# Kernel optimization log

Hardware: AMD Instinct MI355X
Metric: run time of the kernel (lower is better)

## Reference

```python
import jax, jax.numpy as jnp
import numpy as np


def kmax_dmp(x, pool_ranges, k_per, K):
    """Vectorized dynamic k-max pooling (order-preserving top-k along time).

    x: [B, T, C] float. pool_ranges: [B] int (per-sample valid prefix length).
    k_per: [B] int (per-sample k, k_per[i] <= pool_ranges[i]). K: static max k.
    Returns [B, K, C]; rows beyond k_per[i] are zero-padded (like pad_sequence).
    """
    B, T, C = x.shape
    neg = jnp.finfo(x.dtype).min
    valid = jnp.arange(T)[None, :] < pool_ranges[:, None]            # [B,T]
    xm = jnp.where(valid[:, :, None], x, neg)
    vals, idx = jax.lax.top_k(jnp.swapaxes(xm, 1, 2), K)             # [B,C,K]
    keep = jnp.arange(K)[None, None, :] < k_per[:, None, None]       # [B,1,K] bcast
    idx = jnp.where(keep, idx, T)                                    # sentinel for dropped slots
    order = jnp.argsort(idx, axis=-1)                                # restore temporal order
    vals = jnp.take_along_axis(vals, order, axis=-1)
    idx = jnp.take_along_axis(idx, order, axis=-1)
    vals = jnp.where(idx < T, vals, jnp.zeros((), x.dtype))          # zero-pad tail
    return jnp.swapaxes(vals, 1, 2)                                  # [B,K,C]


def setup_inputs() -> dict:
    key = jax.random.key(0)
    ks = jax.random.split(key, 8)
    B, T, C = 64, 512, 300
    x = jax.random.normal(ks[0], (B, T, C), jnp.float32)
    lengths = jnp.sort(jax.random.randint(ks[1], (B,), 16, T + 1))[::-1]
    lengths = lengths.at[0].set(T)  # packed sequences are sorted desc; max len == T
    w1 = jax.random.normal(ks[2], (3 * C, 2, 7), jnp.float32) * 0.05        # groups=C//2 -> 2 in-ch/group
    b1 = jax.random.normal(ks[3], (3 * C,), jnp.float32) * 0.05
    w2 = jax.random.normal(ks[4], (14 * C // 4, 2, 6, 5), jnp.float32) * 0.05  # groups=C//4 -> 2 in-ch/group
    b2 = jax.random.normal(ks[5], (14 * C // 4,), jnp.float32) * 0.05
    wfc = jax.random.normal(ks[6], (1, 4 * 14 * C // 4), jnp.float32) * 0.05
    bfc = jax.random.normal(ks[7], (1,), jnp.float32) * 0.05
    return {"x": x, "lengths": lengths, "w1": w1, "b1": b1,
            "w2": w2, "b2": b2, "wfc": wfc, "bfc": bfc}


def reference(x, lengths, w1, b1, w2, b2, wfc, bfc):
    B, T, C = x.shape
    G1, G2 = C // 2, C // 4
    TOP_K, KS1, KS2W = 4, 7, 5
    # zero out padded tail (pad_packed_sequence semantics)
    mask = (jnp.arange(T)[None, :] < lengths[:, None]).astype(x.dtype)
    x = x * mask[:, :, None]
    # grouped conv1d: [B,C,T] -> [B,3C,T+6]
    h = jax.lax.conv_general_dilated(
        jnp.swapaxes(x, 1, 2), w1, (1,), [(KS1 - 1, KS1 - 1)],
        dimension_numbers=("NCH", "OIH", "NCH"), feature_group_count=G1)
    h = h + b1[None, :, None]
    h = jnp.swapaxes(h, 1, 2)                                       # [B,T+6,3C]
    # layer-1 dynamic k-max: k_i = max(top_k, ceil((2-1)/2 * len_i))
    k1 = jnp.maximum(TOP_K, (lengths + 1) // 2)
    K1 = max(TOP_K, (T + 1) // 2)                                   # static (max len == T)
    h = kmax_dmp(h, lengths + (KS1 - 1), k1, K1)                    # [B,K1,3C]
    h = jnp.tanh(jnp.swapaxes(h, 1, 2).reshape(B, G1, 6, K1))       # [B,C//2,6,K1]
    # grouped conv2d: -> [B,14*C//4,1,K1+4]
    h = jax.lax.conv_general_dilated(
        h, w2, (1, 1), [(0, 0), (KS2W - 1, KS2W - 1)],
        dimension_numbers=("NCHW", "OIHW", "NCHW"), feature_group_count=G2)
    h = h + b2[None, :, None, None]
    Wd = K1 + KS2W - 1
    h = h.reshape(B, G2, 14, Wd).transpose(0, 3, 2, 1)              # [B,Wd,14,C//4]
    h = h.reshape(B, Wd, 14 * G2)
    # layer-2 dynamic k-max: k = top_k = 4; valid prefix = k1 + 4
    h = kmax_dmp(h, k1 + (KS2W - 1), jnp.full((B,), TOP_K, lengths.dtype), TOP_K)
    h = jnp.tanh(h).reshape(B, -1)                                  # [B,4*14*C//4]
    out = h @ wfc.T + bfc                                           # [B,1]
    return jnp.concatenate([jnp.zeros_like(out), out], axis=1)      # [B,2]
```

## Files before the change

kernel.cpp:

```cpp
#include <hip/hip_runtime.h>
#include <cstdint>
#include <cstddef>

#define BB   64
#define TT   512
#define CC   300
#define NG1  150
#define OC1  900
#define L1   518
#define K1   256
#define NG2  75
#define W2LEN 260

__device__ __forceinline__ unsigned f2key(float f) {
    unsigned u = __float_as_uint(f);
    return (u & 0x80000000u) ? ~u : (u | 0x80000000u);
}

__global__ void init_out(const float* __restrict__ bfc, float* __restrict__ out) {
    int i = threadIdx.x;
    if (i < 2 * BB) out[i] = (i & 1) ? bfc[0] : 0.0f;
}

__global__ __launch_bounds__(384) void conv1_kmax(
    const float* __restrict__ x, const int* __restrict__ lengths,
    const float* __restrict__ w1, const float* __restrict__ b1,
    float* __restrict__ y1)
{
    const int g   = blockIdx.x;
    const int b   = blockIdx.y;
    const int tid = threadIdx.x;
    const int len = lengths[b];
    const int n   = len + 6;
    const int k   = max(4, (len + 1) >> 1);

    __shared__ float xs[2][524];
    __shared__ float hrow[6][584];
    __shared__ float ws1[84];
    __shared__ float bs1[6];

    if (tid < 84) ws1[tid] = w1[g * 84 + tid];
    if (tid < 6)  bs1[tid] = b1[g * 6 + tid];

    for (int p = tid; p < 2 * 524; p += 384) {
        int ic = p / 524, q = p - ic * 524;
        int t  = q - 6;
        float v = 0.0f;
        if (t >= 0 && t < len) v = x[((size_t)b * TT + t) * CC + (2 * g + ic)];
        xs[ic][q] = v;
    }
    __syncthreads();

    for (int i = tid; i < 6 * L1; i += 384) {
        int r = i / L1, t = i - r * L1;
        if (t < n) {
            float acc = bs1[r];
            #pragma unroll
            for (int ic = 0; ic < 2; ++ic)
                #pragma unroll
                for (int kk = 0; kk < 7; ++kk)
                    acc = fmaf(xs[ic][t + kk], ws1[r * 14 + ic * 7 + kk], acc);
            hrow[r][t] = acc;
        }
    }
    __syncthreads();

    const int r    = tid >> 6;
    const int lane = tid & 63;

    float    v[9];
    unsigned key[9];
    #pragma unroll
    for (int j = 0; j < 9; ++j) {
        int  t     = lane + 64 * j;
        bool valid = (t < n);
        float vv   = hrow[r][t];
        v[j]   = valid ? vv : 0.0f;
        key[j] = valid ? f2key(vv) : 0u;
    }

    unsigned lo = 1u, hi = 0xFFFFFFFFu;
    while (lo < hi) {
        unsigned mid = lo + ((hi - lo + 1) >> 1);
        int c = 0;
        #pragma unroll
        for (int j = 0; j < 9; ++j) c += (key[j] >= mid) ? 1 : 0;
        for (int o = 32; o; o >>= 1) c += __shfl_xor(c, o);
        if (c >= k) lo = mid; else hi = mid - 1;
    }
    const unsigned tau = lo;

    int cg = 0;
    #pragma unroll
    for (int j = 0; j < 9; ++j) cg += (key[j] > tau) ? 1 : 0;
    for (int o = 32; o; o >>= 1) cg += __shfl_xor(cg, o);
    const int budget = k - cg;

    float* outrow = y1 + ((size_t)(b * OC1 + g * 6 + r)) * K1;
    const unsigned long long below = (1ull << lane) - 1ull;

    int baseG = 0, baseE = 0;
    #pragma unroll
    for (int j = 0; j < 9; ++j) {
        bool isG = key[j] > tau;
        bool isE = (key[j] == tau);
        unsigned long long mG = __ballot(isG);
        unsigned long long mE = __ballot(isE);
        int A = baseG + __popcll(mG & below);
        int E = baseE + __popcll(mE & below);
        if (isG || (isE && E < budget)) {
            int pos = A + (E < budget ? E : budget);
            outrow[pos] = tanhf(v[j]);
        }
        baseG += __popcll(mG);
        baseE += __popcll(mE);
    }
    for (int w = k + lane; w < K1; w += 64) outrow[w] = 0.0f;
}

__global__ __launch_bounds__(256) void conv2_kmax_fc(
    const float* __restrict__ y1, const int* __restrict__ lengths,
    const float* __restrict__ w2, const float* __restrict__ b2,
    const float* __restrict__ wfc, float* __restrict__ out)
{
    const int g   = blockIdx.x;
    const int b   = blockIdx.y;
    const int tid = threadIdx.x;
    const int len = lengths[b];
    const int k1  = max(4, (len + 1) >> 1);
    const int n2  = k1 + 4;

    __shared__ float ys[12][264];
    __shared__ float hs[14][264];
    __shared__ float ws2[14 * 60];
    __shared__ float bs2[14];
    __shared__ float partial[14];

    for (int i = tid; i < 14 * 60; i += 256) ws2[i] = w2[(size_t)g * 840 + i];
    if (tid < 14) bs2[tid] = b2[g * 14 + tid];

    for (int i = tid; i < 12 * 264; i += 256) {
        int c = i / 264, p = i - c * 264;
        int w = p - 4;
        float vv = 0.0f;
        if (w >= 0 && w < K1) vv = y1[((size_t)(b * OC1 + g * 12 + c)) * K1 + w];
        ys[c][p] = vv;
    }
    __syncthreads();

    for (int i = tid; i < 14 * W2LEN; i += 256) {
        int r2 = i / W2LEN, w = i - r2 * W2LEN;
        if (w < n2) {
            float acc = bs2[r2];
            #pragma unroll
            for (int c = 0; c < 12; ++c)
                #pragma unroll
                for (int kw = 0; kw < 5; ++kw)
                    acc = fmaf(ys[c][w + kw], ws2[r2 * 60 + c * 5 + kw], acc);
            hs[r2][w] = acc;
        }
    }
    __syncthreads();

    if (tid < 14) {
        const int r2 = tid;
        float tv0 = -INFINITY, tv1 = -INFINITY, tv2 = -INFINITY, tv3 = -INFINITY;
        int   ti0 = 1 << 30,   ti1 = 1 << 30,   ti2 = 1 << 30,   ti3 = 1 << 30;
        for (int w = 0; w < n2; ++w) {
            float vv = hs[r2][w];
            if (vv > tv3) {
                if (vv > tv0)      { tv3=tv2; ti3=ti2; tv2=tv1; ti2=ti1; tv1=tv0; ti1=ti0; tv0=vv; ti0=w; }
                else if (vv > tv1) { tv3=tv2; ti3=ti2; tv2=tv1; ti2=ti1; tv1=vv; ti1=w; }
                else if (vv > tv2) { tv3=tv2; ti3=ti2; tv2=vv; ti2=w; }
                else               { tv3=vv; ti3=w; }
            }
        }
        #define CSWAP(a,bq) if (ti##a > ti##bq) { int t_=ti##a; ti##a=ti##bq; ti##bq=t_; float f_=tv##a; tv##a=tv##bq; tv##bq=f_; }
        CSWAP(0,1) CSWAP(2,3) CSWAP(0,2) CSWAP(1,3) CSWAP(1,2)
        #undef CSWAP
        const int f = r2 * 75 + g;
        float s = 0.0f;
        s += tanhf(tv0) * wfc[0 * 1050 + f];
        s += tanhf(tv1) * wfc[1 * 1050 + f];
        s += tanhf(tv2) * wfc[2 * 1050 + f];
        s += tanhf(tv3) * wfc[3 * 1050 + f];
        partial[r2] = s;
    }
    __syncthreads();

    if (tid == 0) {
        float s = 0.0f;
        #pragma unroll
        for (int i = 0; i < 14; ++i) s += partial[i];
        atomicAdd(&out[b * 2 + 1], s);
    }
}

extern "C" void kernel_launch(void* const* d_in, const int* in_sizes, int n_in,
                              void* d_out, int out_size, void* d_ws, size_t ws_size,
                              hipStream_t stream) {
    const float* x       = (const float*)d_in[0];
    const int*   lengths = (const int*)  d_in[1];
    const float* w1      = (const float*)d_in[2];
    const float* b1      = (const float*)d_in[3];
    const float* w2      = (const float*)d_in[4];
    const float* b2      = (const float*)d_in[5];
    const float* wfc     = (const float*)d_in[6];
    const float* bfc     = (const float*)d_in[7];
    float* out = (float*)d_out;
    float* y1  = (float*)d_ws;

    init_out<<<dim3(1), dim3(128), 0, stream>>>(bfc, out);
    conv1_kmax<<<dim3(NG1, BB), dim3(384), 0, stream>>>(x, lengths, w1, b1, y1);
    conv2_kmax_fc<<<dim3(NG2, BB), dim3(256), 0, stream>>>(y1, lengths, w2, b2, wfc, out);
}
```

Measured before the change: 397.7 us.

## Register-resident conv1/conv2 with float-bisection k-max and wave-parallel top-4 selection

Conv1 now computes each output row in registers, with every lane handling S consecutive timesteps loaded via float4. The k-max threshold is found by bisection on float values bounded by the row min and max, with an early exit, instead of a 32-step bisection over integer keys. Conv2 drops its shared-memory staging: each wave loads padded y1 rows (stride 264, zero-padded) straight from global memory and accumulates 4 outputs × 4 channels in registers. Its top-4 selection becomes a wave-wide argmax reduction instead of serial selection on 14 threads. Fast tanh approximations and per-wave atomics reduce the remaining overhead, at some precision risk and more atomic traffic.

Measured after the change: 335.1 us. -15.7%, faster.

```diff
diff --git a/kernel.cpp b/kernel.cpp
--- a/kernel.cpp
+++ b/kernel.cpp
@@ -7,19 +7,143 @@
 #define CC   300
 #define NG1  150
 #define OC1  900
-#define L1   518
 #define K1   256
+#define RS   264
 #define NG2  75
-#define W2LEN 260
 
 __device__ __forceinline__ unsigned f2key(float f) {
     unsigned u = __float_as_uint(f);
     return (u & 0x80000000u) ? ~u : (u | 0x80000000u);
 }
+__device__ __forceinline__ float key2f(unsigned k) {
+    unsigned u = (k & 0x80000000u) ? (k & 0x7FFFFFFFu) : ~k;
+    return __uint_as_float(u);
+}
+__device__ __forceinline__ float fast_tanh(float x) {
+    float e = __expf(2.0f * x);
+    return 1.0f - 2.0f * __builtin_amdgcn_rcpf(e + 1.0f);
+}
+__device__ __forceinline__ int mbcnt64(unsigned long long m) {
+    return (int)__builtin_amdgcn_mbcnt_hi((unsigned)(m >> 32),
+                 __builtin_amdgcn_mbcnt_lo((unsigned)m, 0u));
+}
 
 __global__ void init_out(const float* __restrict__ bfc, float* __restrict__ out) {
     int i = threadIdx.x;
     if (i < 2 * BB) out[i] = (i & 1) ? bfc[0] : 0.0f;
+}
+
+template<int S>
+__device__ __forceinline__ void conv1_core(
+    const float (* __restrict__ xs)[524], int lane, int n, int k,
+    const float* wA, const float* wB, float br, float* __restrict__ row)
+{
+    constexpr int NV = (S == 8) ? 16 : 12;
+    const int t0 = S * lane;
+
+    float xa[NV], xb[NV];
+    #pragma unroll
+    for (int q = 0; q < NV / 4; ++q) {
+        *(float4*)&xa[4 * q] = *(const float4*)&xs[0][t0 + 4 * q];
+        *(float4*)&xb[4 * q] = *(const float4*)&xs[1][t0 + 4 * q];
+    }
+
+    float v[S + 1];
+    #pragma unroll
+    for (int j = 0; j < S; ++j) {
+        float acc = br;
+        #pragma unroll
+        for (int kk = 0; kk < 7; ++kk)
+            acc = fmaf(xa[j + kk], wA[kk], fmaf(xb[j + kk], wB[kk], acc));
+        v[j] = (t0 + j < n) ? acc : -INFINITY;
+    }
+    v[S] = -INFINITY;
+    if (S == 8 && n > 512) {
+        if (lane < 6 && 512 + lane < n) {
+            float acc = br;
+            #pragma unroll
+            for (int kk = 0; kk < 7; ++kk)
+                acc = fmaf(xs[0][512 + lane + kk], wA[kk],
+                      fmaf(xs[1][512 + lane + kk], wB[kk], acc));
+            v[S] = acc;
+        }
+    }
+
+    float lmax = -INFINITY, lmin = INFINITY;
+    #pragma unroll
+    for (int j = 0; j <= S; ++j) {
+        lmax = fmaxf(lmax, v[j]);
+        lmin = fminf(lmin, (v[j] == -INFINITY) ? INFINITY : v[j]);
+    }
+    #pragma unroll
+    for (int o = 32; o; o >>= 1) {
+        lmax = fmaxf(lmax, __shfl_xor(lmax, o));
+        lmin = fminf(lmin, __shfl_xor(lmin, o));
+    }
+    const float vmax = lmax, vmin = lmin;
+
+    float tau; bool found = false;
+    int cmax = 0;
+    #pragma unroll
+    for (int j = 0; j <= S; ++j) cmax += (int)__popcll(__ballot(v[j] == vmax));
+    if (cmax >= k) {
+        tau = vmax;
+    } else {
+        float lo = vmin, hi = vmax;
+        tau = lo;
+        while (true) {
+            float mid = 0.5f * (lo + hi);
+            if (mid == lo || mid == hi) { tau = lo; break; }
+            int c = 0;
+            #pragma unroll
+            for (int j = 0; j <= S; ++j)
+                c += (int)__popcll(__ballot(v[j] >= mid));
+            if (c == k) { tau = mid; found = true; break; }
+            if (c > k) lo = mid; else hi = mid;
+        }
+    }
+
+    bool bG[S + 1], bE[S + 1];
+    unsigned long long mG[S + 1], mE[S + 1];
+    #pragma unroll
+    for (int j = 0; j <= S; ++j) {
+        bG[j] = found ? (v[j] >= tau) : (v[j] > tau);
+        bE[j] = found ? false : (v[j] == tau);
+        mG[j] = __ballot(bG[j]);
+        mE[j] = __ballot(bE[j]);
+    }
+    int cg = 0;
+    #pragma unroll
+    for (int j = 0; j <= S; ++j) cg += (int)__popcll(mG[j]);
+    const int budget = k - cg;
+
+    int SGm = 0, SEm = 0, FGm = 0, FEm = 0;
+    #pragma unroll
+    for (int j = 0; j < S; ++j) {
+        SGm += mbcnt64(mG[j]);  FGm += (int)__popcll(mG[j]);
+        SEm += mbcnt64(mE[j]);  FEm += (int)__popcll(mE[j]);
+    }
+    int ownG = 0, ownE = 0;
+    #pragma unroll
+    for (int j = 0; j < S; ++j) {
+        if (bG[j] || bE[j]) {
+            int E = SEm + ownE;
+            if (bG[j] || E < budget) {
+                int pos = SGm + ownG + min(E, budget);
+                row[4 + pos] = fast_tanh(v[j]);
+            }
+        }
+        ownG += bG[j] ? 1 : 0;  ownE += bE[j] ? 1 : 0;
+    }
+    if (S == 8 && (bG[S] || bE[S])) {
+        int E = FEm + mbcnt64(mE[S]);
+        if (bG[S] || E < budget) {
+            int pos = FGm + mbcnt64(mG[S]) + min(E, budget);
+            row[4 + pos] = fast_tanh(v[S]);
+        }
+    }
+    if (lane < 4) row[lane] = 0.0f;
+    for (int w = k + lane; w < RS - 4; w += 64) row[4 + w] = 0.0f;
 }
 
 __global__ __launch_bounds__(384) void conv1_kmax(
@@ -27,95 +151,34 @@
     const float* __restrict__ w1, const float* __restrict__ b1,
     float* __restrict__ y1)
 {
-    const int g   = blockIdx.x;
-    const int b   = blockIdx.y;
+    const int g = blockIdx.x, b = blockIdx.y;
     const int tid = threadIdx.x;
     const int len = lengths[b];
-    const int n   = len + 6;
-    const int k   = max(4, (len + 1) >> 1);
-
-    __shared__ float xs[2][524];
-    __shared__ float hrow[6][584];
-    __shared__ float ws1[84];
-    __shared__ float bs1[6];
-
-    if (tid < 84) ws1[tid] = w1[g * 84 + tid];
-    if (tid < 6)  bs1[tid] = b1[g * 6 + tid];
-
-    for (int p = tid; p < 2 * 524; p += 384) {
-        int ic = p / 524, q = p - ic * 524;
-        int t  = q - 6;
-        float v = 0.0f;
-        if (t >= 0 && t < len) v = x[((size_t)b * TT + t) * CC + (2 * g + ic)];
-        xs[ic][q] = v;
+    const int n = len + 6;
+    const int k = max(4, (len + 1) >> 1);
+
+    __shared__ __align__(16) float xs[2][524];
+    __shared__ float ws[84];
+    __shared__ float bs[6];
+    if (tid < 84) ws[tid] = w1[g * 84 + tid];
+    if (tid < 6)  bs[tid] = b1[g * 6 + tid];
+    for (int p = tid; p < 1048; p += 384) {
+        int ic = (p >= 524) ? 1 : 0;
+        int q = p - ic * 524;
+        int t = q - 6;
+        xs[ic][q] = (t >= 0 && t < len) ? x[((size_t)b * TT + t) * CC + 2 * g + ic] : 0.0f;
     }
     __syncthreads();
 
-    for (int i = tid; i < 6 * L1; i += 384) {
-        int r = i / L1, t = i - r * L1;
-        if (t < n) {
-            float acc = bs1[r];
-            #pragma unroll
-            for (int ic = 0; ic < 2; ++ic)
-                #pragma unroll
-                for (int kk = 0; kk < 7; ++kk)
-                    acc = fmaf(xs[ic][t + kk], ws1[r * 14 + ic * 7 + kk], acc);
-            hrow[r][t] = acc;
-        }
-    }
-    __syncthreads();
-
-    const int r    = tid >> 6;
-    const int lane = tid & 63;
-
-    float    v[9];
-    unsigned key[9];
-    #pragma unroll
-    for (int j = 0; j < 9; ++j) {
-        int  t     = lane + 64 * j;
-        bool valid = (t < n);
-        float vv   = hrow[r][t];
-        v[j]   = valid ? vv : 0.0f;
-        key[j] = valid ? f2key(vv) : 0u;
-    }
-
-    unsigned lo = 1u, hi = 0xFFFFFFFFu;
-    while (lo < hi) {
-        unsigned mid = lo + ((hi - lo + 1) >> 1);
-        int c = 0;
-        #pragma unroll
-        for (int j = 0; j < 9; ++j) c += (key[j] >= mid) ? 1 : 0;
-        for (int o = 32; o; o >>= 1) c += __shfl_xor(c, o);
-        if (c >= k) lo = mid; else hi = mid - 1;
-    }
-    const unsigned tau = lo;
-
-    int cg = 0;
-    #pragma unroll
-    for (int j = 0; j < 9; ++j) cg += (key[j] > tau) ? 1 : 0;
-    for (int o = 32; o; o >>= 1) cg += __shfl_xor(cg, o);
-    const int budget = k - cg;
-
-    float* outrow = y1 + ((size_t)(b * OC1 + g * 6 + r)) * K1;
-    const unsigned long long below = (1ull << lane) - 1ull;
-
-    int baseG = 0, baseE = 0;
-    #pragma unroll
-    for (int j = 0; j < 9; ++j) {
-        bool isG = key[j] > tau;
-        bool isE = (key[j] == tau);
-        unsigned long long mG = __ballot(isG);
-        unsigned long long mE = __ballot(isE);
-        int A = baseG + __popcll(mG & below);
-        int E = baseE + __popcll(mE & below);
-        if (isG || (isE && E < budget)) {
-            int pos = A + (E < budget ? E : budget);
-            outrow[pos] = tanhf(v[j]);
-        }
-        baseG += __popcll(mG);
-        baseE += __popcll(mE);
-    }
-    for (int w = k + lane; w < K1; w += 64) outrow[w] = 0.0f;
+    const int r = tid >> 6, lane = tid & 63;
+    float wA[7], wB[7];
+    #pragma unroll
+    for (int i = 0; i < 7; ++i) { wA[i] = ws[r * 14 + i]; wB[i] = ws[r * 14 + 7 + i]; }
+    const float br = bs[r];
+    float* row = y1 + ((size_t)b * OC1 + g * 6 + r) * RS;
+
+    if (n <= 256) conv1_core<4>(xs, lane, n, k, wA, wB, br, row);
+    else          conv1_core<8>(xs, lane, n, k, wA, wB, br, row);
 }
 
 __global__ __launch_bounds__(256) void conv2_kmax_fc(
@@ -123,77 +186,128 @@
     const float* __restrict__ w2, const float* __restrict__ b2,
     const float* __restrict__ wfc, float* __restrict__ out)
 {
-    const int g   = blockIdx.x;
-    const int b   = blockIdx.y;
+    const int g = blockIdx.x, b = blockIdx.y;
     const int tid = threadIdx.x;
+    const int wv = tid >> 6, lane = tid & 63;
     const int len = lengths[b];
-    const int k1  = max(4, (len + 1) >> 1);
-    const int n2  = k1 + 4;
-
-    __shared__ float ys[12][264];
-    __shared__ float hs[14][264];
-    __shared__ float ws2[14 * 60];
-    __shared__ float bs2[14];
-    __shared__ float partial[14];
-
-    for (int i = tid; i < 14 * 60; i += 256) ws2[i] = w2[(size_t)g * 840 + i];
-    if (tid < 14) bs2[tid] = b2[g * 14 + tid];
-
-    for (int i = tid; i < 12 * 264; i += 256) {
-        int c = i / 264, p = i - c * 264;
-        int w = p - 4;
-        float vv = 0.0f;
-        if (w >= 0 && w < K1) vv = y1[((size_t)(b * OC1 + g * 12 + c)) * K1 + w];
-        ys[c][p] = vv;
-    }
-    __syncthreads();
-
-    for (int i = tid; i < 14 * W2LEN; i += 256) {
-        int r2 = i / W2LEN, w = i - r2 * W2LEN;
-        if (w < n2) {
-            float acc = bs2[r2];
-            #pragma unroll
-            for (int c = 0; c < 12; ++c)
-                #pragma unroll
-                for (int kw = 0; kw < 5; ++kw)
-                    acc = fmaf(ys[c][w + kw], ws2[r2 * 60 + c * 5 + kw], acc);
-            hs[r2][w] = acc;
-        }
-    }
-    __syncthreads();
-
-    if (tid < 14) {
-        const int r2 = tid;
-        float tv0 = -INFINITY, tv1 = -INFINITY, tv2 = -INFINITY, tv3 = -INFINITY;
-        int   ti0 = 1 << 30,   ti1 = 1 << 30,   ti2 = 1 << 30,   ti3 = 1 << 30;
-        for (int w = 0; w < n2; ++w) {
-            float vv = hs[r2][w];
-            if (vv > tv3) {
-                if (vv > tv0)      { tv3=tv2; ti3=ti2; tv2=tv1; ti2=ti1; tv1=tv0; ti1=ti0; tv0=vv; ti0=w; }
-                else if (vv > tv1) { tv3=tv2; ti3=ti2; tv2=tv1; ti2=ti1; tv1=vv; ti1=w; }
-                else if (vv > tv2) { tv3=tv2; ti3=ti2; tv2=vv; ti2=w; }
-                else               { tv3=vv; ti3=w; }
+    const int k1 = max(4, (len + 1) >> 1);
+    const int n2 = k1 + 4;
+
+    const int r2u0 = __builtin_amdgcn_readfirstlane(4 * wv);
+    const int nch  = (wv == 3) ? 2 : 4;
+    const float* __restrict__ wg = w2 + (size_t)g * 840;
+    const float* base = y1 + ((size_t)b * OC1 + g * 12) * RS;
+
+    float bias_s[4];
+    #pragma unroll
+    for (int it = 0; it < 4; ++it)
+        bias_s[it] = (4 * wv + it < 14) ? b2[(size_t)g * 14 + r2u0 + it] : 0.0f;
+
+    float acc[4][4];
+    #pragma unroll
+    for (int it = 0; it < 4; ++it)
+        #pragma unroll
+        for (int j = 0; j < 4; ++j) acc[it][j] = bias_s[it];
+
+    for (int c = 0; c < 12; ++c) {
+        const float* rp = base + (size_t)c * RS;
+        const float4 f0 = *(const float4*)&rp[4 * lane];
+        const float4 f1 = *(const float4*)&rp[4 * lane + 4];
+        const float e[8] = {f0.x, f0.y, f0.z, f0.w, f1.x, f1.y, f1.z, f1.w};
+        #pragma unroll
+        for (int it = 0; it < 4; ++it) {
+            if (it < nch) {
+                const float* wp = wg + (r2u0 + it) * 60 + c * 5;
+                #pragma unroll
+                for (int kw = 0; kw < 5; ++kw) {
+                    const float q = wp[kw];
+                    acc[it][0] = fmaf(e[0 + kw], q, acc[it][0]);
+                    acc[it][1] = fmaf(e[1 + kw], q, acc[it][1]);
+                    acc[it][2] = fmaf(e[2 + kw], q, acc[it][2]);
+                    acc[it][3] = fmaf(e[3 + kw], q, acc[it][3]);
+                }
             }
         }
-        #define CSWAP(a,bq) if (ti##a > ti##bq) { int t_=ti##a; ti##a=ti##bq; ti##bq=t_; float f_=tv##a; tv##a=tv##bq; tv##bq=f_; }
-        CSWAP(0,1) CSWAP(2,3) CSWAP(0,2) CSWAP(1,3) CSWAP(1,2)
-        #undef CSWAP
-        const int f = r2 * 75 + g;
-        float s = 0.0f;
-        s += tanhf(tv0) * wfc[0 * 1050 + f];
-        s += tanhf(tv1) * wfc[1 * 1050 + f];
-        s += tanhf(tv2) * wfc[2 * 1050 + f];
-        s += tanhf(tv3) * wfc[3 * 1050 + f];
-        partial[r2] = s;
-    }
-    __syncthreads();
-
-    if (tid == 0) {
-        float s = 0.0f;
-        #pragma unroll
-        for (int i = 0; i < 14; ++i) s += partial[i];
-        atomicAdd(&out[b * 2 + 1], s);
-    }
+    }
+
+    float tval[4];
+    #pragma unroll
+    for (int it = 0; it < 4; ++it) tval[it] = -INFINITY;
+    if (n2 > 256) {
+        if (lane < 4 && 256 + lane < n2) {
+            const int w = 256 + lane;
+            float ta[4];
+            #pragma unroll
+            for (int it = 0; it < 4; ++it) ta[it] = bias_s[it];
+            for (int c = 0; c < 12; ++c) {
+                const float* rp = base + (size_t)c * RS;
+                #pragma unroll
+                for (int kw = 0; kw < 5; ++kw) {
+                    const float xv = rp[w + kw];
+                    #pragma unroll
+                    for (int it = 0; it < 4; ++it)
+                        if (it < nch)
+                            ta[it] = fmaf(xv, wg[(r2u0 + it) * 60 + c * 5 + kw], ta[it]);
+                }
+            }
+            #pragma unroll
+            for (int it = 0; it < 4; ++it) tval[it] = ta[it];
+        }
+    }
+
+    float fcsum = 0.0f;
+    #pragma unroll
+    for (int it = 0; it < 4; ++it) {
+        if (it < nch) {
+            unsigned kk[5];
+            #pragma unroll
+            for (int j = 0; j < 4; ++j)
+                kk[j] = (4 * lane + j < n2) ? f2key(acc[it][j]) : 0u;
+            kk[4] = (tval[it] != -INFINITY) ? f2key(tval[it]) : 0u;
+
+            float tv[4]; int ti[4];
+            #pragma unroll
+            for (int round = 0; round < 4; ++round) {
+                unsigned best = max(max(kk[0], kk[1]), max(kk[2], kk[3]));
+                best = max(best, kk[4]);
+                #pragma unroll
+                for (int o = 32; o; o >>= 1)
+                    best = max(best, (unsigned)__shfl_xor((int)best, o));
+                int jm = 5;
+                #pragma unroll
+                for (int j = 4; j >= 0; --j) if (kk[j] == best) jm = j;
+                unsigned long long m = __ballot(jm < 5);
+                int wl;
+                if (__popcll(m) == 1) {
+                    wl = __ffsll((long long)m) - 1;
+                } else {
+                    int myt = (jm == 4) ? (256 + lane)
+                            : (jm < 4 ? 4 * lane + jm : 0x7FFFFFFF);
+                    int tmin = myt;
+                    #pragma unroll
+                    for (int o = 32; o; o >>= 1) tmin = min(tmin, __shfl_xor(tmin, o));
+                    wl = __ffsll((long long)__ballot(myt == tmin)) - 1;
+                }
+                const int jw = __shfl(jm, wl);
+                ti[round] = (jw == 4) ? (256 + wl) : (4 * wl + jw);
+                tv[round] = key2f(best);
+                #pragma unroll
+                for (int j = 0; j < 5; ++j)
+                    if (lane == wl && jm == j) kk[j] = 0u;
+            }
+            #define CSW(a,bq) if (ti[a] > ti[bq]) { int t_=ti[a]; ti[a]=ti[bq]; ti[bq]=t_; float f_=tv[a]; tv[a]=tv[bq]; tv[bq]=f_; }
+            CSW(0,1) CSW(2,3) CSW(0,2) CSW(1,3) CSW(1,2)
+            #undef CSW
+
+            const float* wfp = wfc + (r2u0 + it) * 75 + g;
+            float s = fast_tanh(tv[0]) * wfp[0];
+            s = fmaf(fast_tanh(tv[1]), wfp[1050], s);
+            s = fmaf(fast_tanh(tv[2]), wfp[2100], s);
+            s = fmaf(fast_tanh(tv[3]), wfp[3150], s);
+            fcsum += s;
+        }
+    }
+    if (lane == 0) atomicAdd(&out[b * 2 + 1], fcsum);
 }
 
 extern "C" void kernel_launch(void* const* d_in, const int* in_sizes, int n_in,
```
